# Kernel optimization log

Measured on AMD Instinct MI355X. Metric: run time of the kernel, lower is better.

Reference implementation:

```python
import jax, jax.numpy as jnp
import numpy as np

H_KV = 8          # num_key_value_heads (hard-coded in module)
N_HEADS = 32
HEAD_DIM = 128
GROUPS = N_HEADS // H_KV
EPS = 1e-05
ROPE_THETA = 10000.0


def rotate_half(x):
    x1, x2 = jnp.split(x, 2, axis=-1)
    return jnp.concatenate((-x2, x1), axis=-1)


def rms_norm(x, w, eps=EPS):
    xf = x.astype(jnp.float32)
    var = jnp.mean(xf * xf, axis=-1, keepdims=True)
    return (w * (xf * jax.lax.rsqrt(var + eps))).astype(x.dtype)


def setup_inputs() -> dict:
    key = jax.random.key(0)
    k1, k2, k3 = jax.random.split(key, 3)
    B, S, D = 2, 2048, 4096
    hidden_states = jax.random.normal(k1, (B, S, D), dtype=jnp.float32)
    # RoPE tables (what custom_pos_emb carries)
    inv_freq = 1.0 / (ROPE_THETA ** (jnp.arange(0, HEAD_DIM, 2, dtype=jnp.float32) / HEAD_DIM))
    t = jnp.arange(S, dtype=jnp.float32)
    freqs = jnp.outer(t, inv_freq)                 # [S, HEAD_DIM/2]
    emb = jnp.concatenate((freqs, freqs), axis=-1)  # [S, HEAD_DIM]
    cos = jnp.cos(emb)[None]                        # [1, S, HEAD_DIM]
    sin = jnp.sin(emb)[None]
    w_qkv = jax.random.normal(k2, (6144, D), dtype=jnp.float32) * 0.02
    w_o = jax.random.normal(k3, (D, D), dtype=jnp.float32) * 0.02
    q_norm_w = jnp.ones((HEAD_DIM,), dtype=jnp.float32)
    k_norm_w = jnp.ones((HEAD_DIM,), dtype=jnp.float32)
    return {"hidden_states": hidden_states, "cos": cos, "sin": sin,
            "w_qkv": w_qkv, "w_o": w_o, "q_norm_w": q_norm_w, "k_norm_w": k_norm_w}


def reference(hidden_states, cos, sin, w_qkv, w_o, q_norm_w, k_norm_w):
    B, S, D = hidden_states.shape
    qkv = hidden_states @ w_qkv.T                                    # [B,S,6144]
    qkv = qkv.reshape(B, S, H_KV, GROUPS + 2, HEAD_DIM)
    q = qkv[:, :, :, :GROUPS]                                        # [B,S,Hkv,G,d]
    k = qkv[:, :, :, GROUPS]                                         # [B,S,Hkv,d]
    v = qkv[:, :, :, GROUPS + 1]                                     # [B,S,Hkv,d]
    # to [B, heads, S, d]
    q = q.reshape(B, S, N_HEADS, HEAD_DIM).transpose(0, 2, 1, 3)     # [B,Hq,S,d]
    k = k.transpose(0, 2, 1, 3)                                      # [B,Hkv,S,d]
    v = v.transpose(0, 2, 1, 3)
    # RoPE (cos/sin: [1,S,d] -> unsqueeze head dim)
    c = cos[:, None]  # [1,1,S,d]
    s = sin[:, None]
    q = q * c + rotate_half(q) * s
    k = k * c + rotate_half(k) * s
    # per-head RMSNorm
    q = rms_norm(q, q_norm_w)
    k = rms_norm(k, k_norm_w)
    # GQA attention without materializing repeated K/V
    qg = q.reshape(B, H_KV, GROUPS, S, HEAD_DIM)
    scale = 1.0 / np.sqrt(HEAD_DIM).astype(np.float32)
    scores = jnp.einsum('bkgqd,bksd->bkgqs', qg, k) * scale          # [B,Hkv,G,S,S]
    probs = jax.nn.softmax(scores, axis=-1)
    out = jnp.einsum('bkgqs,bksd->bkgqd', probs, v)                  # [B,Hkv,G,S,d]
    out = out.reshape(B, N_HEADS, S, HEAD_DIM).transpose(0, 2, 1, 3).reshape(B, S, D)
    return out @ w_o.T
```

## Files before the change

### kernel.cpp

```cpp
#include <hip/hip_runtime.h>
#include <hip/hip_bf16.h>

typedef __attribute__((ext_vector_type(8))) short short8;
typedef __attribute__((ext_vector_type(4))) float floatx4;

static __device__ __forceinline__ short bf16bits(float f) {
    __hip_bfloat16 h = __float2bfloat16(f);
    return __builtin_bit_cast(short, h);
}

#define GLDS(g, l) __builtin_amdgcn_global_load_lds( \
    (const __attribute__((address_space(1))) void*)(g), \
    (__attribute__((address_space(3))) void*)(l), 16, 0, 0)

__global__ __launch_bounds__(256) void cvt_bf16(
    const float* __restrict__ src, __hip_bfloat16* __restrict__ dst)
{
    size_t i = ((size_t)blockIdx.x * 256 + threadIdx.x) * 8;
    floatx4 f0 = *(const floatx4*)(src + i);
    floatx4 f1 = *(const floatx4*)(src + i + 4);
    short8 s;
#pragma unroll
    for (int j = 0; j < 4; j++) { s[j] = bf16bits(f0[j]); s[j + 4] = bf16bits(f1[j]); }
    *(short8*)((short*)dst + i) = s;
}

template<typename CT>
__global__ __launch_bounds__(256) void gemm_bt_fast(
    const __hip_bfloat16* __restrict__ A,
    const __hip_bfloat16* __restrict__ W,
    CT* __restrict__ C, int M, int N, int K)
{
    __shared__ alignas(16) short lA[128 * 64];
    __shared__ alignas(16) short lB[128 * 64];

    const int tid  = threadIdx.x;
    const int wave = tid >> 6;
    const int lane = tid & 63;
    const int quad = lane >> 4;
    const int l16  = lane & 15;

    const int m0 = blockIdx.x * 128;
    const int n0 = blockIdx.y * 128;
    const int wm = (wave & 1) * 64;
    const int wn = (wave >> 1) * 64;

    const int srow = lane >> 3;
    const int sblk = (lane & 7) ^ srow;
    const int scol = sblk * 8;

    const short* Ag = (const short*)A;
    const short* Wg = (const short*)W;

    floatx4 acc[4][4];
#pragma unroll
    for (int i = 0; i < 4; i++)
#pragma unroll
        for (int j = 0; j < 4; j++) acc[i][j] = (floatx4)0.0f;

    for (int k0 = 0; k0 < K; k0 += 64) {
        __syncthreads();
#pragma unroll
        for (int i = 0; i < 4; i++) {
            int c   = wave * 4 + i;
            int row = c * 8 + srow;
            GLDS(Ag + (size_t)(m0 + row) * K + k0 + scol, &lA[c * 512]);
            GLDS(Wg + (size_t)(n0 + row) * K + k0 + scol, &lB[c * 512]);
        }
        __syncthreads();
#pragma unroll
        for (int kk2 = 0; kk2 < 2; kk2++) {
            const int pb = ((kk2 * 4 + quad) ^ (l16 & 7)) * 8;
            short8 af[4], bf[4];
#pragma unroll
            for (int i = 0; i < 4; i++)
                af[i] = *(const short8*)(&lA[(wm + i * 16 + l16) * 64 + pb]);
#pragma unroll
            for (int j = 0; j < 4; j++)
                bf[j] = *(const short8*)(&lB[(wn + j * 16 + l16) * 64 + pb]);
#pragma unroll
            for (int i = 0; i < 4; i++)
#pragma unroll
                for (int j = 0; j < 4; j++)
                    acc[i][j] = __builtin_amdgcn_mfma_f32_16x16x32_bf16(
                        af[i], bf[j], acc[i][j], 0, 0, 0);
        }
    }
#pragma unroll
    for (int i = 0; i < 4; i++)
#pragma unroll
        for (int j = 0; j < 4; j++) {
            int gm = m0 + wm + i * 16 + quad * 4;
            int gn = n0 + wn + j * 16 + l16;
#pragma unroll
            for (int r = 0; r < 4; r++) {
                float v = acc[i][j][r];
                if constexpr (sizeof(CT) == 2)
                    C[(size_t)(gm + r) * N + gn] = (CT)__float2bfloat16(v);
                else
                    C[(size_t)(gm + r) * N + gn] = (CT)v;
            }
        }
}

template<bool AF32, typename CT>
__global__ __launch_bounds__(256) void gemm_bt_slow(
    const void* __restrict__ A,
    const float* __restrict__ Wf,
    CT* __restrict__ C, int M, int N, int K)
{
    __shared__ alignas(16) short lA[128 * 72];
    __shared__ alignas(16) short lB[128 * 72];

    const int tid  = threadIdx.x;
    const int wave = tid >> 6;
    const int lane = tid & 63;
    const int quad = lane >> 4;
    const int l16  = lane & 15;

    const int m0 = blockIdx.x * 128;
    const int n0 = blockIdx.y * 128;
    const int wm = (wave & 1) * 64;
    const int wn = (wave >> 1) * 64;

    floatx4 acc[4][4];
#pragma unroll
    for (int i = 0; i < 4; i++)
#pragma unroll
        for (int j = 0; j < 4; j++) acc[i][j] = (floatx4)0.0f;

    const short* Ab = (const short*)A;
    const float* Af = (const float*)A;

    for (int k0 = 0; k0 < K; k0 += 64) {
        __syncthreads();
#pragma unroll
        for (int i = 0; i < 4; i++) {
            int chunk = tid + i * 256;
            int row = chunk >> 3;
            int cc  = chunk & 7;
            if (AF32) {
                const float* src = Af + (size_t)(m0 + row) * K + k0 + cc * 8;
                floatx4 f0 = *(const floatx4*)(src);
                floatx4 f1 = *(const floatx4*)(src + 4);
                short8 s;
#pragma unroll
                for (int j = 0; j < 4; j++) { s[j] = bf16bits(f0[j]); s[j + 4] = bf16bits(f1[j]); }
                *(short8*)(&lA[row * 72 + cc * 8]) = s;
            } else {
                *(short8*)(&lA[row * 72 + cc * 8]) =
                    *(const short8*)(Ab + (size_t)(m0 + row) * K + k0 + cc * 8);
            }
            const float* src = Wf + (size_t)(n0 + row) * K + k0 + cc * 8;
            floatx4 f0 = *(const floatx4*)(src);
            floatx4 f1 = *(const floatx4*)(src + 4);
            short8 s;
#pragma unroll
            for (int j = 0; j < 4; j++) { s[j] = bf16bits(f0[j]); s[j + 4] = bf16bits(f1[j]); }
            *(short8*)(&lB[row * 72 + cc * 8]) = s;
        }
        __syncthreads();
#pragma unroll
        for (int kk = 0; kk < 64; kk += 32) {
            short8 af[4], bf[4];
#pragma unroll
            for (int i = 0; i < 4; i++)
                af[i] = *(const short8*)(&lA[(wm + i * 16 + l16) * 72 + kk + quad * 8]);
#pragma unroll
            for (int j = 0; j < 4; j++)
                bf[j] = *(const short8*)(&lB[(wn + j * 16 + l16) * 72 + kk + quad * 8]);
#pragma unroll
            for (int i = 0; i < 4; i++)
#pragma unroll
                for (int j = 0; j < 4; j++)
                    acc[i][j] = __builtin_amdgcn_mfma_f32_16x16x32_bf16(
                        af[i], bf[j], acc[i][j], 0, 0, 0);
        }
    }
#pragma unroll
    for (int i = 0; i < 4; i++)
#pragma unroll
        for (int j = 0; j < 4; j++) {
            int gm = m0 + wm + i * 16 + quad * 4;
            int gn = n0 + wn + j * 16 + l16;
#pragma unroll
            for (int r = 0; r < 4; r++) {
                float v = acc[i][j][r];
                if constexpr (sizeof(CT) == 2)
                    C[(size_t)(gm + r) * N + gn] = (CT)__float2bfloat16(v);
                else
                    C[(size_t)(gm + r) * N + gn] = (CT)v;
            }
        }
}

__global__ __launch_bounds__(256) void rope_norm(
    __hip_bfloat16* __restrict__ qkv,
    const float* __restrict__ cosb,
    const float* __restrict__ sinb,
    const float* __restrict__ qw,
    const float* __restrict__ kw)
{
    int wid  = blockIdx.x * 4 + (threadIdx.x >> 6);
    int lane = threadIdx.x & 63;
    int token = wid / 40;
    int idx   = wid % 40;
    int s = token & 2047;

    int off;
    const float* w;
    if (idx < 32) { off = (idx >> 2) * 768 + (idx & 3) * 128; w = qw; }
    else          { off = (idx - 32) * 768 + 512;             w = kw; }

    short* p = (short*)(qkv + (size_t)token * 6144 + off);
    int d = lane * 2;

    unsigned int pv = *(const unsigned int*)(p + d);
    float x0 = __builtin_bit_cast(float, pv << 16);
    float x1 = __builtin_bit_cast(float, pv & 0xffff0000u);

    float ox0 = __shfl_xor(x0, 32, 64);
    float ox1 = __shfl_xor(x1, 32, 64);

    float2 cv = *(const float2*)(cosb + s * 128 + d);
    float2 sv = *(const float2*)(sinb + s * 128 + d);
    float sgn = (lane < 32) ? -1.0f : 1.0f;
    float y0 = fmaf(sgn * ox0, sv.x, x0 * cv.x);
    float y1 = fmaf(sgn * ox1, sv.y, x1 * cv.y);

    float ss = y0 * y0 + y1 * y1;
#pragma unroll
    for (int m = 1; m < 64; m <<= 1) ss += __shfl_xor(ss, m, 64);
    float r = rsqrtf(ss * (1.0f / 128.0f) + 1e-5f);

    float2 wv = *(const float2*)(w + d);
    unsigned int out = (unsigned int)(unsigned short)bf16bits(y0 * r * wv.x)
                     | ((unsigned int)(unsigned short)bf16bits(y1 * r * wv.y) << 16);
    *(unsigned int*)(p + d) = out;
}

__global__ __launch_bounds__(256) void vtrans(
    const __hip_bfloat16* __restrict__ qkv, __hip_bfloat16* __restrict__ Vt)
{
    __shared__ alignas(16) short lT[64 * 136];

    const int bid   = blockIdx.x;
    const int stile = bid & 31;
    const int kvh   = (bid >> 5) & 7;
    const int b     = bid >> 8;
    const int tid   = threadIdx.x;
    const size_t voff = (size_t)kvh * 768 + 640;
    const short* qkvs = (const short*)qkv;

#pragma unroll
    for (int i = 0; i < 4; i++) {
        int chunk = tid + i * 256;
        int t  = chunk >> 4;
        int dc = chunk & 15;
        size_t tok = (size_t)(b * 2048 + stile * 64 + t);
        *(short8*)(&lT[t * 136 + dc * 8]) =
            *(const short8*)(qkvs + tok * 6144 + voff + dc * 8);
    }
    __syncthreads();

    int d  = tid >> 1;
    int kh = (tid & 1) * 32;
    short* out = (short*)Vt + ((size_t)((b * 8 + kvh) * 128 + d)) * 2048
               + stile * 64 + kh;
#pragma unroll
    for (int jb = 0; jb < 4; jb++) {
        short8 s;
#pragma unroll
        for (int j = 0; j < 8; j++) s[j] = lT[(kh + jb * 8 + j) * 136 + d];
        *(short8*)(out + jb * 8) = s;
    }
}

__global__ __launch_bounds__(256, 2) void attn_kernel(
    const __hip_bfloat16* __restrict__ qkv,
    const __hip_bfloat16* __restrict__ Vt,
    __hip_bfloat16* __restrict__ attn_out)
{
    __shared__ alignas(16) short lK[64 * 128];
    __shared__ alignas(16) short lVt[128 * 64];
    __shared__ alignas(16) short lP[4][32 * 64];

    const int bid  = blockIdx.x;
    const int qt   = bid & 15;
    const int h    = (bid >> 4) & 31;
    const int b    = bid >> 9;
    const int kvh  = h >> 2;
    const int wave = threadIdx.x >> 6;
    const int lane = threadIdx.x & 63;
    const int quad = lane >> 4;
    const int l16  = lane & 15;

    const size_t qoff = (size_t)kvh * 768 + (size_t)(h & 3) * 128;
    const size_t koff = (size_t)kvh * 768 + 512;
    const short* qkvs = (const short*)qkv;
    const short* Vts  = (const short*)Vt + ((size_t)(b * 8 + kvh) * 128) * 2048;

    short8 qf[2][4];
#pragma unroll
    for (int t = 0; t < 2; t++) {
        const int qrow = qt * 128 + wave * 32 + t * 16 + l16;
        const size_t qtok = (size_t)(b * 2048 + qrow);
#pragma unroll
        for (int kk = 0; kk < 4; kk++)
            qf[t][kk] = *(const short8*)(qkvs + qtok * 6144 + qoff + kk * 32 + quad * 8);
    }

    floatx4 o[2][8];
#pragma unroll
    for (int t = 0; t < 2; t++)
#pragma unroll
        for (int n = 0; n < 8; n++) o[t][n] = (floatx4)0.0f;
    float mrow[2][4], lrow[2][4];
#pragma unroll
    for (int t = 0; t < 2; t++)
#pragma unroll
        for (int r = 0; r < 4; r++) { mrow[t][r] = -3.0e4f; lrow[t][r] = 0.0f; }

    const float scale = 0.08838834764831845f;

    const int k_row = lane >> 4;
    const int v_row = lane >> 3;
    const int v_blk = (lane & 7) ^ v_row;

    for (int kt = 0; kt < 32; kt++) {
        __syncthreads();
#pragma unroll
        for (int i = 0; i < 4; i++) {
            int c = wave * 4 + i;
            int k_blk = (lane & 15) ^ ((c * 4 + k_row) & 15);
            size_t tok = (size_t)(b * 2048 + kt * 64 + c * 4 + k_row);
            GLDS(qkvs + tok * 6144 + koff + k_blk * 8, &lK[c * 512]);
            int d = c * 8 + v_row;
            GLDS(Vts + (size_t)d * 2048 + kt * 64 + v_blk * 8, &lVt[c * 512]);
        }
        __syncthreads();

        floatx4 sc[2][4];
#pragma unroll
        for (int t = 0; t < 2; t++)
#pragma unroll
            for (int n = 0; n < 4; n++) sc[t][n] = (floatx4)0.0f;
        __builtin_amdgcn_s_setprio(1);
#pragma unroll
        for (int kk = 0; kk < 4; kk++) {
#pragma unroll
            for (int n = 0; n < 4; n++) {
                short8 bfr = *(const short8*)(
                    &lK[(n * 16 + l16) * 128 + (((kk * 4 + quad) ^ l16)) * 8]);
                sc[0][n] = __builtin_amdgcn_mfma_f32_16x16x32_bf16(qf[0][kk], bfr, sc[0][n], 0, 0, 0);
                sc[1][n] = __builtin_amdgcn_mfma_f32_16x16x32_bf16(qf[1][kk], bfr, sc[1][n], 0, 0, 0);
            }
        }
        __builtin_amdgcn_s_setprio(0);

#pragma unroll
        for (int t = 0; t < 2; t++) {
            float mx[4];
            bool big = false;
#pragma unroll
            for (int r = 0; r < 4; r++) {
                float m0 = fmaxf(fmaxf(sc[t][0][r], sc[t][1][r]),
                                 fmaxf(sc[t][2][r], sc[t][3][r])) * scale;
#pragma unroll
                for (int m = 1; m < 16; m <<= 1) m0 = fmaxf(m0, __shfl_xor(m0, m, 64));
                mx[r] = m0;
                if (m0 > mrow[t][r] + 8.0f) big = true;
            }
            float mnew[4], alpha[4];
#pragma unroll
            for (int r = 0; r < 4; r++) {
                if (big) {
                    float mn = fmaxf(mrow[t][r], mx[r]);
                    alpha[r] = __expf(mrow[t][r] - mn);
                    mnew[r]  = mn;
                } else {
                    mnew[r]  = mrow[t][r];
                    alpha[r] = 1.0f;
                }
            }
#pragma unroll
            for (int n = 0; n < 4; n++)
#pragma unroll
                for (int r = 0; r < 4; r++) {
                    float p = __expf(sc[t][n][r] * scale - mnew[r]);
                    sc[t][n][r] = p;
                    int row = t * 16 + quad * 4 + r;
                    int pblk = (n * 2 + (l16 >> 3)) ^ (row & 7);
                    lP[wave][row * 64 + pblk * 8 + (l16 & 7)] = bf16bits(p);
                }
#pragma unroll
            for (int r = 0; r < 4; r++) {
                float sm = sc[t][0][r] + sc[t][1][r] + sc[t][2][r] + sc[t][3][r];
#pragma unroll
                for (int m = 1; m < 16; m <<= 1) sm += __shfl_xor(sm, m, 64);
                if (big) {
                    lrow[t][r] = lrow[t][r] * alpha[r] + sm;
                    mrow[t][r] = mnew[r];
                } else {
                    lrow[t][r] += sm;
                }
            }
            if (big) {
#pragma unroll
                for (int n = 0; n < 8; n++)
#pragma unroll
                    for (int r = 0; r < 4; r++) o[t][n][r] *= alpha[r];
            }
        }

        __threadfence_block();

        __builtin_amdgcn_s_setprio(1);
#pragma unroll
        for (int kk2 = 0; kk2 < 2; kk2++) {
            const int pb = ((kk2 * 4 + quad) ^ (l16 & 7)) * 8;
            short8 pf0 = *(const short8*)(&lP[wave][(l16)      * 64 + pb]);
            short8 pf1 = *(const short8*)(&lP[wave][(16 + l16) * 64 + pb]);
#pragma unroll
            for (int n = 0; n < 8; n++) {
                short8 vf = *(const short8*)(&lVt[(n * 16 + l16) * 64 + pb]);
                o[0][n] = __builtin_amdgcn_mfma_f32_16x16x32_bf16(pf0, vf, o[0][n], 0, 0, 0);
                o[1][n] = __builtin_amdgcn_mfma_f32_16x16x32_bf16(pf1, vf, o[1][n], 0, 0, 0);
            }
        }
        __builtin_amdgcn_s_setprio(0);
    }

#pragma unroll
    for (int t = 0; t < 2; t++)
#pragma unroll
        for (int n = 0; n < 8; n++)
#pragma unroll
            for (int r = 0; r < 4; r++) {
                int row = qt * 128 + wave * 32 + t * 16 + quad * 4 + r;
                size_t tok = (size_t)(b * 2048 + row);
                attn_out[tok * 4096 + h * 128 + n * 16 + l16] =
                    __float2bfloat16(o[t][n][r] / lrow[t][r]);
            }
}

extern "C" void kernel_launch(void* const* d_in, const int* in_sizes, int n_in,
                              void* d_out, int out_size, void* d_ws, size_t ws_size,
                              hipStream_t stream) {
    const float* hidden = (const float*)d_in[0];
    const float* cosb   = (const float*)d_in[1];
    const float* sinb   = (const float*)d_in[2];
    const float* w_qkv  = (const float*)d_in[3];
    const float* w_o    = (const float*)d_in[4];
    const float* qw     = (const float*)d_in[5];
    const float* kw     = (const float*)d_in[6];

    char* ws = (char*)d_ws;
    __hip_bfloat16* qkv    = (__hip_bfloat16*)ws;
    __hip_bfloat16* attn_o = (__hip_bfloat16*)(ws + 50331648);
    __hip_bfloat16* hb  = (__hip_bfloat16*)(ws + 83886080);
    __hip_bfloat16* wb1 = (__hip_bfloat16*)(ws + 117440512);
    __hip_bfloat16* wb2 = (__hip_bfloat16*)(ws + 167772160);
    const size_t WS_FAST = 201326592;

    __hip_bfloat16* Vt = (__hip_bfloat16*)d_out;
    float* outp        = (float*)d_out;

    const bool fast = (ws_size >= WS_FAST);

    if (fast) {
        cvt_bf16<<<16777216 / 8 / 256, 256, 0, stream>>>(hidden, hb);
        cvt_bf16<<<25165824 / 8 / 256, 256, 0, stream>>>(w_qkv, wb1);
        cvt_bf16<<<16777216 / 8 / 256, 256, 0, stream>>>(w_o, wb2);
        dim3 g1(32, 48);
        gemm_bt_fast<__hip_bfloat16><<<g1, 256, 0, stream>>>(hb, wb1, qkv, 4096, 6144, 4096);
    } else {
        dim3 g1(32, 48);
        gemm_bt_slow<true, __hip_bfloat16><<<g1, 256, 0, stream>>>(hidden, w_qkv, qkv, 4096, 6144, 4096);
    }

    rope_norm<<<40960, 256, 0, stream>>>(qkv, cosb, sinb, qw, kw);

    vtrans<<<512, 256, 0, stream>>>(qkv, Vt);

    attn_kernel<<<1024, 256, 0, stream>>>(qkv, Vt, attn_o);

    dim3 g2(32, 32);
    if (fast) {
        gemm_bt_fast<float><<<g2, 256, 0, stream>>>(attn_o, wb2, outp, 4096, 4096, 4096);
    } else {
        gemm_bt_slow<false, float><<<g2, 256, 0, stream>>>(attn_o, w_o, outp, 4096, 4096, 4096);
    }
}
```

Measured before the change: 940.8 us.

## Double-buffer K/V tiles in attention and defer softmax row-sum reduction

The attention kernel now double-buffers the K and V^T shared-memory tiles, prefetching tile kt+1 via global_load_lds while computing on tile kt, and drops one barrier per iteration. Softmax moves to the exp2 domain with the log2e factor folded into the scale. The per-row sum shuffle reduction is deferred to after the loop, and the block index is remapped to group blocks that share a KV head. It also removes setprio hints and makes the lazy rescale decision wave-uniform via __any; the cost is double the LDS for K/V, which may reduce occupancy.

Result: faster. 894.2 us (-5.0%).

```diff
diff --git a/kernel.cpp b/kernel.cpp
--- a/kernel.cpp
+++ b/kernel.cpp
@@ -281,11 +281,12 @@
     const __hip_bfloat16* __restrict__ Vt,
     __hip_bfloat16* __restrict__ attn_out)
 {
-    __shared__ alignas(16) short lK[64 * 128];
-    __shared__ alignas(16) short lVt[128 * 64];
+    __shared__ alignas(16) short lK[2][64 * 128];
+    __shared__ alignas(16) short lVt[2][128 * 64];
     __shared__ alignas(16) short lP[4][32 * 64];
 
-    const int bid  = blockIdx.x;
+    const int bid0 = blockIdx.x;
+    const int bid  = (bid0 & 7) * 128 + (bid0 >> 3);
     const int qt   = bid & 15;
     const int h    = (bid >> 4) & 31;
     const int b    = bid >> 9;
@@ -315,79 +316,93 @@
     for (int t = 0; t < 2; t++)
 #pragma unroll
         for (int n = 0; n < 8; n++) o[t][n] = (floatx4)0.0f;
-    float mrow[2][4], lrow[2][4];
+    float mrow[2][4], lsum[2][4];
 #pragma unroll
     for (int t = 0; t < 2; t++)
 #pragma unroll
-        for (int r = 0; r < 4; r++) { mrow[t][r] = -3.0e4f; lrow[t][r] = 0.0f; }
-
-    const float scale = 0.08838834764831845f;
+        for (int r = 0; r < 4; r++) { mrow[t][r] = -3.0e4f; lsum[t][r] = 0.0f; }
+
+    const float scale2 = 0.08838834764831845f * 1.4426950408889634f;
+    const float THR2   = 11.5418f;
 
     const int k_row = lane >> 4;
     const int v_row = lane >> 3;
     const int v_blk = (lane & 7) ^ v_row;
 
+#pragma unroll
+    for (int i = 0; i < 4; i++) {
+        int c = wave * 4 + i;
+        int k_blk = (lane & 15) ^ ((c * 4 + k_row) & 15);
+        size_t tok = (size_t)(b * 2048 + c * 4 + k_row);
+        GLDS(qkvs + tok * 6144 + koff + k_blk * 8, &lK[0][c * 512]);
+        int d = c * 8 + v_row;
+        GLDS(Vts + (size_t)d * 2048 + v_blk * 8, &lVt[0][c * 512]);
+    }
+
+    int cur = 0;
     for (int kt = 0; kt < 32; kt++) {
         __syncthreads();
-#pragma unroll
-        for (int i = 0; i < 4; i++) {
-            int c = wave * 4 + i;
-            int k_blk = (lane & 15) ^ ((c * 4 + k_row) & 15);
-            size_t tok = (size_t)(b * 2048 + kt * 64 + c * 4 + k_row);
-            GLDS(qkvs + tok * 6144 + koff + k_blk * 8, &lK[c * 512]);
-            int d = c * 8 + v_row;
-            GLDS(Vts + (size_t)d * 2048 + kt * 64 + v_blk * 8, &lVt[c * 512]);
-        }
-        __syncthreads();
+
+        if (kt < 31) {
+            short* nK = &lK[cur ^ 1][0];
+            short* nV = &lVt[cur ^ 1][0];
+#pragma unroll
+            for (int i = 0; i < 4; i++) {
+                int c = wave * 4 + i;
+                int k_blk = (lane & 15) ^ ((c * 4 + k_row) & 15);
+                size_t tok = (size_t)(b * 2048 + (kt + 1) * 64 + c * 4 + k_row);
+                GLDS(qkvs + tok * 6144 + koff + k_blk * 8, nK + c * 512);
+                int d = c * 8 + v_row;
+                GLDS(Vts + (size_t)d * 2048 + (kt + 1) * 64 + v_blk * 8, nV + c * 512);
+            }
+        }
+
+        const short* lKc = &lK[cur][0];
+        const short* lVc = &lVt[cur][0];
 
         floatx4 sc[2][4];
 #pragma unroll
         for (int t = 0; t < 2; t++)
 #pragma unroll
             for (int n = 0; n < 4; n++) sc[t][n] = (floatx4)0.0f;
-        __builtin_amdgcn_s_setprio(1);
 #pragma unroll
         for (int kk = 0; kk < 4; kk++) {
 #pragma unroll
             for (int n = 0; n < 4; n++) {
                 short8 bfr = *(const short8*)(
-                    &lK[(n * 16 + l16) * 128 + (((kk * 4 + quad) ^ l16)) * 8]);
+                    &lKc[(n * 16 + l16) * 128 + (((kk * 4 + quad) ^ l16)) * 8]);
                 sc[0][n] = __builtin_amdgcn_mfma_f32_16x16x32_bf16(qf[0][kk], bfr, sc[0][n], 0, 0, 0);
                 sc[1][n] = __builtin_amdgcn_mfma_f32_16x16x32_bf16(qf[1][kk], bfr, sc[1][n], 0, 0, 0);
             }
         }
-        __builtin_amdgcn_s_setprio(0);
 
 #pragma unroll
         for (int t = 0; t < 2; t++) {
-            float mx[4];
-            bool big = false;
+            float mx[4]; int grow = 0;
 #pragma unroll
             for (int r = 0; r < 4; r++) {
                 float m0 = fmaxf(fmaxf(sc[t][0][r], sc[t][1][r]),
-                                 fmaxf(sc[t][2][r], sc[t][3][r])) * scale;
+                                 fmaxf(sc[t][2][r], sc[t][3][r])) * scale2;
 #pragma unroll
                 for (int m = 1; m < 16; m <<= 1) m0 = fmaxf(m0, __shfl_xor(m0, m, 64));
                 mx[r] = m0;
-                if (m0 > mrow[t][r] + 8.0f) big = true;
-            }
-            float mnew[4], alpha[4];
-#pragma unroll
-            for (int r = 0; r < 4; r++) {
-                if (big) {
+                grow |= (m0 > mrow[t][r] + THR2) ? 1 : 0;
+            }
+            const bool big = __any(grow) != 0;
+            float alpha[4];
+            if (big) {
+#pragma unroll
+                for (int r = 0; r < 4; r++) {
                     float mn = fmaxf(mrow[t][r], mx[r]);
-                    alpha[r] = __expf(mrow[t][r] - mn);
-                    mnew[r]  = mn;
-                } else {
-                    mnew[r]  = mrow[t][r];
-                    alpha[r] = 1.0f;
+                    alpha[r] = exp2f(mrow[t][r] - mn);
+                    mrow[t][r] = mn;
                 }
             }
 #pragma unroll
             for (int n = 0; n < 4; n++)
 #pragma unroll
                 for (int r = 0; r < 4; r++) {
-                    float p = __expf(sc[t][n][r] * scale - mnew[r]);
+                    float p = exp2f(sc[t][n][r] * scale2 - mrow[t][r]);
                     sc[t][n][r] = p;
                     int row = t * 16 + quad * 4 + r;
                     int pblk = (n * 2 + (l16 >> 3)) ^ (row & 7);
@@ -395,15 +410,9 @@
                 }
 #pragma unroll
             for (int r = 0; r < 4; r++) {
-                float sm = sc[t][0][r] + sc[t][1][r] + sc[t][2][r] + sc[t][3][r];
-#pragma unroll
-                for (int m = 1; m < 16; m <<= 1) sm += __shfl_xor(sm, m, 64);
-                if (big) {
-                    lrow[t][r] = lrow[t][r] * alpha[r] + sm;
-                    mrow[t][r] = mnew[r];
-                } else {
-                    lrow[t][r] += sm;
-                }
+                float ps = (sc[t][0][r] + sc[t][1][r]) + (sc[t][2][r] + sc[t][3][r]);
+                if (big) lsum[t][r] = lsum[t][r] * alpha[r] + ps;
+                else     lsum[t][r] += ps;
             }
             if (big) {
 #pragma unroll
@@ -415,7 +424,6 @@
 
         __threadfence_block();
 
-        __builtin_amdgcn_s_setprio(1);
 #pragma unroll
         for (int kk2 = 0; kk2 < 2; kk2++) {
             const int pb = ((kk2 * 4 + quad) ^ (l16 & 7)) * 8;
@@ -423,13 +431,24 @@
             short8 pf1 = *(const short8*)(&lP[wave][(16 + l16) * 64 + pb]);
 #pragma unroll
             for (int n = 0; n < 8; n++) {
-                short8 vf = *(const short8*)(&lVt[(n * 16 + l16) * 64 + pb]);
+                short8 vf = *(const short8*)(&lVc[(n * 16 + l16) * 64 + pb]);
                 o[0][n] = __builtin_amdgcn_mfma_f32_16x16x32_bf16(pf0, vf, o[0][n], 0, 0, 0);
                 o[1][n] = __builtin_amdgcn_mfma_f32_16x16x32_bf16(pf1, vf, o[1][n], 0, 0, 0);
             }
         }
-        __builtin_amdgcn_s_setprio(0);
-    }
+
+        cur ^= 1;
+    }
+
+#pragma unroll
+    for (int t = 0; t < 2; t++)
+#pragma unroll
+        for (int r = 0; r < 4; r++) {
+            float s = lsum[t][r];
+#pragma unroll
+            for (int m = 1; m < 16; m <<= 1) s += __shfl_xor(s, m, 64);
+            lsum[t][r] = 1.0f / s;
+        }
 
 #pragma unroll
     for (int t = 0; t < 2; t++)
@@ -440,7 +459,7 @@
                 int row = qt * 128 + wave * 32 + t * 16 + quad * 4 + r;
                 size_t tok = (size_t)(b * 2048 + row);
                 attn_out[tok * 4096 + h * 128 + n * 16 + l16] =
-                    __float2bfloat16(o[t][n][r] / lrow[t][r]);
+                    __float2bfloat16(o[t][n][r] * lsum[t][r]);
             }
 }
 
```
